# Kernel optimization log

Hardware: AMD Instinct MI355X
Metric: run time of the kernel (lower is better)

## Reference

```python
import jax, jax.numpy as jnp
import numpy as np

TOP_K = 2

def setup_inputs() -> dict:
    key = jax.random.key(0)
    k1, k2 = jax.random.split(key)
    x = jax.random.normal(k1, (8, 4096, 4096), dtype=jnp.float32)
    # nn.Linear weight [num_experts, dim]
    gate_w = jax.random.normal(k2, (64, 4096), dtype=jnp.float32) * (1.0 / np.sqrt(4096))
    return {"x": x, "gate_w": gate_w}

def reference(x, gate_w):
    # logits: [B, S, E]
    logits = jnp.einsum('bsd,ed->bse', x, gate_w)
    routing_weights = jax.nn.softmax(logits, axis=-1)
    top_weights, top_indices = jax.lax.top_k(routing_weights, TOP_K)
    top_weights = top_weights / jnp.sum(top_weights, axis=-1, keepdims=True)
    return top_weights, top_indices
```

## Files before the change

### kernel.cpp

```cpp
#include <hip/hip_runtime.h>
#include <hip/hip_bf16.h>
#include <math.h>


typedef __attribute__((ext_vector_type(8))) short short8;
typedef __attribute__((ext_vector_type(4))) float f32x4;

#define TPB 32
#define NCH 32
#define TAU 1e-4f
#define LROW 68

__device__ __forceinline__ void cvt8(const f32x4* v, short8* hi, short8* lo) {
    const float* f = reinterpret_cast<const float*>(v);
#pragma unroll
    for (int j = 0; j < 8; ++j) {
        __hip_bfloat16 h = __float2bfloat16(f[j]);
        float r = f[j] - __bfloat162float(h);
        __hip_bfloat16 l = __float2bfloat16(r);
        (*hi)[j] = (short)*reinterpret_cast<unsigned short*>(&h);
        (*lo)[j] = (short)*reinterpret_cast<unsigned short*>(&l);
    }
}

__global__ void prep_b(const float* __restrict__ gw,
                       short8* __restrict__ bh, short8* __restrict__ bl) {
    const int tid = blockIdx.x * 256 + threadIdx.x;
    const int ln  = tid & 63;
    const int w   = (tid >> 6) & 127;
    const int nt  = tid >> 13;
    const int row = nt * 16 + (ln & 15);
    const int k   = w * 32 + ((ln >> 4) << 3);
    f32x4 v[2];
    v[0] = *reinterpret_cast<const f32x4*>(gw + (long)row * 4096 + k);
    v[1] = *reinterpret_cast<const f32x4*>(gw + (long)row * 4096 + k + 4);
    short8 h, l;
    cvt8(v, &h, &l);
    bh[tid] = h;
    bl[tid] = l;
}

__device__ __forceinline__ void gload16(const void* g, void* l) {
    __builtin_amdgcn_global_load_lds(
        (const __attribute__((address_space(1))) void*)g,
        (__attribute__((address_space(3))) void*)l, 16, 0, 0);
}

#define STAGE(C, BUF) do {                                                    \
    char* aB = AB + (BUF) * 16384;                                            \
    _Pragma("unroll")                                                         \
    for (int i = 0; i < 4; ++i)                                               \
        gload16(srcA[i] + (long)(C) * 512, aB + (wv * 4 + i) * 1024 + ln * 16); \
} while (0)

__global__ __launch_bounds__(256, 4)
void router_fused(const float* __restrict__ x,
                  const short8* __restrict__ bhp,
                  const short8* __restrict__ blp,
                  const float* __restrict__ gw,
                  float* __restrict__ out,
                  int M, int K) {
    __shared__ __align__(16) char AB[32768];
    __shared__ int flags[TPB];
    __shared__ double Ld4[4][64];

    const int t  = threadIdx.x;
    const int wv = t >> 6;
    const int ln = t & 63;
    const int fr = ln & 15;
    const int q  = ln >> 4;
    const int mm = wv >> 1;
    const int nn = wv & 1;
    const long tok0 = (long)blockIdx.x * TPB;
    const int phase = blockIdx.x & (NCH - 1);

    const char* srcA[4];
#pragma unroll
    for (int i = 0; i < 4; ++i) {
        const int row  = 2 * (wv * 4 + i) + (ln >> 5);
        const int slot = (ln & 31);
        const int swz  = (slot & ~7) | ((slot & 7) ^ (row & 7));
        srcA[i] = (const char*)x + (tok0 + row) * (long)K * 4 + swz * 16;
    }

    f32x4 acc[2];
    acc[0] = (f32x4){0.f, 0.f, 0.f, 0.f};
    acc[1] = (f32x4){0.f, 0.f, 0.f, 0.f};

    STAGE(phase, 0);
    STAGE((phase + 1) & (NCH - 1), 1);

    const int R = mm * 16 + fr;
    const int rk = R & 7;

    for (int j = 0; j < NCH; ++j) {
        const int c   = (phase + j) & (NCH - 1);
        const int buf = j & 1;
        if (j + 1 < NCH) asm volatile("s_waitcnt vmcnt(4)" ::: "memory");
        else             asm volatile("s_waitcnt vmcnt(0)" ::: "memory");
        __builtin_amdgcn_s_barrier();
        asm volatile("" ::: "memory");
        __builtin_amdgcn_sched_barrier(0);

        {
            const char* aB = AB + buf * 16384 + R * 512;
#pragma unroll
            for (int w = 0; w < 4; ++w) {
                f32x4 av[2];
                av[0] = *(const f32x4*)(aB + (w * 8 + ((q * 2 + 0) ^ rk)) * 16);
                av[1] = *(const f32x4*)(aB + (w * 8 + ((q * 2 + 1) ^ rk)) * 16);
                short8 ah, al;
                cvt8(av, &ah, &al);
                const int widx = c * 4 + w;
#pragma unroll
                for (int ntl = 0; ntl < 2; ++ntl) {
                    const int nt = 2 * nn + ntl;
                    short8 bhv = bhp[nt * 8192 + widx * 64 + ln];
                    short8 blv = blp[nt * 8192 + widx * 64 + ln];
                    acc[ntl] = __builtin_amdgcn_mfma_f32_16x16x32_bf16(ah, bhv, acc[ntl], 0, 0, 0);
                    acc[ntl] = __builtin_amdgcn_mfma_f32_16x16x32_bf16(ah, blv, acc[ntl], 0, 0, 0);
                    acc[ntl] = __builtin_amdgcn_mfma_f32_16x16x32_bf16(al, bhv, acc[ntl], 0, 0, 0);
                    acc[ntl] = __builtin_amdgcn_mfma_f32_16x16x32_bf16(al, blv, acc[ntl], 0, 0, 0);
                }
            }
        }

        __builtin_amdgcn_sched_barrier(0);
        asm volatile("" ::: "memory");
        __builtin_amdgcn_s_barrier();
        asm volatile("" ::: "memory");
        if (j + 2 < NCH) STAGE((phase + j + 2) & (NCH - 1), buf);
        __builtin_amdgcn_sched_barrier(0);
    }

    __syncthreads();
    float* Ls = (float*)AB;
#pragma unroll
    for (int ntl = 0; ntl < 2; ++ntl)
#pragma unroll
        for (int r = 0; r < 4; ++r)
            Ls[(mm * 16 + q * 4 + r) * LROW + (2 * nn + ntl) * 16 + fr] = acc[ntl][r];
    __syncthreads();

    if (t < TPB) {
        const float* row = Ls + (long)t * LROW;
        float m1 = -INFINITY, m2 = -INFINITY, m3 = -INFINITY;
        int i1 = 0, i2 = 0;
#pragma unroll 8
        for (int e = 0; e < 64; ++e) {
            const float v = row[e];
            if (v > m1)      { m3 = m2; m2 = m1; i2 = i1; m1 = v; i1 = e; }
            else if (v > m2) { m3 = m2; m2 = v; i2 = e; }
            else if (v > m3) { m3 = v; }
        }
        const float e2 = expf(m2 - m1);
        const float s  = 1.0f + e2;

        const long g = tok0 + t;
        out[2 * g + 0] = 1.0f / s;
        out[2 * g + 1] = e2 / s;
        float* oi = out + 2 * (long)M;
        oi[2 * g + 0] = (float)i1;
        oi[2 * g + 1] = (float)i2;

        flags[t] = ((m1 - m2) < TAU) | ((m2 - m3) < TAU);
    }
    __syncthreads();

    for (int tk = 0; tk < TPB; ++tk) {
        if (flags[tk]) {
            const float* xr = x + (tok0 + tk) * (long)K + wv * 1024;
            const float* gr = gw + (long)ln * (long)K + wv * 1024;
            double s0 = 0.0, s1 = 0.0, s2 = 0.0, s3 = 0.0;
            for (int k = 0; k < 1024; k += 4) {
                const f32x4 a = *reinterpret_cast<const f32x4*>(xr + k);
                const f32x4 b = *reinterpret_cast<const f32x4*>(gr + k);
                s0 = fma((double)a.x, (double)b.x, s0);
                s1 = fma((double)a.y, (double)b.y, s1);
                s2 = fma((double)a.z, (double)b.z, s2);
                s3 = fma((double)a.w, (double)b.w, s3);
            }
            Ld4[wv][ln] = (s0 + s1) + (s2 + s3);
            __syncthreads();
            if (t == 0) {
                double m1 = -INFINITY, m2 = -INFINITY;
                int i1 = 0, i2 = 0;
                for (int e = 0; e < 64; ++e) {
                    const double v = Ld4[0][e] + Ld4[1][e] + Ld4[2][e] + Ld4[3][e];
                    if (v > m1)      { m2 = m1; i2 = i1; m1 = v; i1 = e; }
                    else if (v > m2) { m2 = v; i2 = e; }
                }
                const double e2 = exp(m2 - m1);
                const double s  = 1.0 + e2;
                const long g = tok0 + tk;
                out[2 * g + 0] = (float)(1.0 / s);
                out[2 * g + 1] = (float)(e2 / s);
                float* oi = out + 2 * (long)M;
                oi[2 * g + 0] = (float)i1;
                oi[2 * g + 1] = (float)i2;
            }
            __syncthreads();
        }
    }
}

extern "C" void kernel_launch(void* const* d_in, const int* in_sizes, int n_in,
                              void* d_out, int out_size, void* d_ws, size_t ws_size,
                              hipStream_t stream) {
    const float* x  = (const float*)d_in[0];
    const float* gw = (const float*)d_in[1];
    float* out = (float*)d_out;

    const int K = 4096;
    const int M = in_sizes[0] / K;
    const int nblocks = M / TPB;

    short8* bh = (short8*)d_ws;
    short8* bl = bh + 32768;

    prep_b<<<128, 256, 0, stream>>>(gw, bh, bl);
    router_fused<<<nblocks, 256, 0, stream>>>(x, bh, bl, gw, out, M, K);
}
```

Before: 233.1 us.

## Stage B weights through LDS and widen block to 64 tokens

```diff
diff --git a/kernel.cpp b/kernel.cpp
--- a/kernel.cpp
+++ b/kernel.cpp
@@ -6,8 +6,8 @@
 typedef __attribute__((ext_vector_type(8))) short short8;
 typedef __attribute__((ext_vector_type(4))) float f32x4;
 
-#define TPB 32
-#define NCH 32
+#define TPB 64
+#define NCH 64
 #define TAU 1e-4f
 #define LROW 68
 
@@ -47,20 +47,29 @@
 }
 
 #define STAGE(C, BUF) do {                                                    \
-    char* aB = AB + (BUF) * 16384;                                            \
+    char* aB = AB + (BUF) * 32768;                                            \
+    char* bB = aB + 16384;                                                    \
     _Pragma("unroll")                                                         \
     for (int i = 0; i < 4; ++i)                                               \
-        gload16(srcA[i] + (long)(C) * 512, aB + (wv * 4 + i) * 1024 + ln * 16); \
+        gload16(srcA[i] + (long)(C) * 256, aB + (wv * 4 + i) * 1024 + ln * 16); \
+    _Pragma("unroll")                                                         \
+    for (int i = 0; i < 4; ++i) {                                             \
+        const int s  = wv * 4 + i;                                            \
+        const int wl = s >> 3, nt = (s >> 1) & 3, hl = s & 1;                 \
+        const short8* sp = (hl ? blp : bhp)                                   \
+            + ((long)nt * 8192 + (2 * (C) + wl) * 64 + ln);                   \
+        gload16(sp, bB + s * 1024 + ln * 16);                                 \
+    }                                                                         \
 } while (0)
 
-__global__ __launch_bounds__(256, 4)
+__global__ __launch_bounds__(256, 2)
 void router_fused(const float* __restrict__ x,
                   const short8* __restrict__ bhp,
                   const short8* __restrict__ blp,
                   const float* __restrict__ gw,
                   float* __restrict__ out,
                   int M, int K) {
-    __shared__ __align__(16) char AB[32768];
+    __shared__ __align__(16) char AB[65536];
     __shared__ int flags[TPB];
     __shared__ double Ld4[4][64];
 
@@ -69,58 +78,55 @@
     const int ln = t & 63;
     const int fr = ln & 15;
     const int q  = ln >> 4;
-    const int mm = wv >> 1;
-    const int nn = wv & 1;
     const long tok0 = (long)blockIdx.x * TPB;
     const int phase = blockIdx.x & (NCH - 1);
 
     const char* srcA[4];
 #pragma unroll
     for (int i = 0; i < 4; ++i) {
-        const int row  = 2 * (wv * 4 + i) + (ln >> 5);
-        const int slot = (ln & 31);
-        const int swz  = (slot & ~7) | ((slot & 7) ^ (row & 7));
-        srcA[i] = (const char*)x + (tok0 + row) * (long)K * 4 + swz * 16;
-    }
-
-    f32x4 acc[2];
-    acc[0] = (f32x4){0.f, 0.f, 0.f, 0.f};
-    acc[1] = (f32x4){0.f, 0.f, 0.f, 0.f};
+        const int row  = (wv * 4 + i) * 4 + (ln >> 4);
+        const int sl   = ln & 15;
+        const int lslot = (sl & 8) | ((sl & 7) ^ (row & 7));
+        srcA[i] = (const char*)x + (tok0 + row) * (long)K * 4 + lslot * 16;
+    }
+
+    f32x4 acc[4];
+#pragma unroll
+    for (int nt = 0; nt < 4; ++nt) acc[nt] = (f32x4){0.f, 0.f, 0.f, 0.f};
 
     STAGE(phase, 0);
     STAGE((phase + 1) & (NCH - 1), 1);
 
-    const int R = mm * 16 + fr;
+    const int R  = wv * 16 + fr;
     const int rk = R & 7;
 
     for (int j = 0; j < NCH; ++j) {
         const int c   = (phase + j) & (NCH - 1);
         const int buf = j & 1;
-        if (j + 1 < NCH) asm volatile("s_waitcnt vmcnt(4)" ::: "memory");
+        if (j + 1 < NCH) asm volatile("s_waitcnt vmcnt(8)" ::: "memory");
         else             asm volatile("s_waitcnt vmcnt(0)" ::: "memory");
         __builtin_amdgcn_s_barrier();
         asm volatile("" ::: "memory");
         __builtin_amdgcn_sched_barrier(0);
 
         {
-            const char* aB = AB + buf * 16384 + R * 512;
-#pragma unroll
-            for (int w = 0; w < 4; ++w) {
+            const char* aB = AB + buf * 32768 + R * 256;
+            const char* bB = AB + buf * 32768 + 16384;
+#pragma unroll
+            for (int wl = 0; wl < 2; ++wl) {
                 f32x4 av[2];
-                av[0] = *(const f32x4*)(aB + (w * 8 + ((q * 2 + 0) ^ rk)) * 16);
-                av[1] = *(const f32x4*)(aB + (w * 8 + ((q * 2 + 1) ^ rk)) * 16);
+                av[0] = *(const f32x4*)(aB + (wl * 8 + ((q * 2 + 0) ^ rk)) * 16);
+                av[1] = *(const f32x4*)(aB + (wl * 8 + ((q * 2 + 1) ^ rk)) * 16);
                 short8 ah, al;
                 cvt8(av, &ah, &al);
-                const int widx = c * 4 + w;
-#pragma unroll
-                for (int ntl = 0; ntl < 2; ++ntl) {
-                    const int nt = 2 * nn + ntl;
-                    short8 bhv = bhp[nt * 8192 + widx * 64 + ln];
-                    short8 blv = blp[nt * 8192 + widx * 64 + ln];
-                    acc[ntl] = __builtin_amdgcn_mfma_f32_16x16x32_bf16(ah, bhv, acc[ntl], 0, 0, 0);
-                    acc[ntl] = __builtin_amdgcn_mfma_f32_16x16x32_bf16(ah, blv, acc[ntl], 0, 0, 0);
-                    acc[ntl] = __builtin_amdgcn_mfma_f32_16x16x32_bf16(al, bhv, acc[ntl], 0, 0, 0);
-                    acc[ntl] = __builtin_amdgcn_mfma_f32_16x16x32_bf16(al, blv, acc[ntl], 0, 0, 0);
+#pragma unroll
+                for (int nt = 0; nt < 4; ++nt) {
+                    short8 bhv = *(const short8*)(bB + (wl * 8 + nt * 2 + 0) * 1024 + ln * 16);
+                    short8 blv = *(const short8*)(bB + (wl * 8 + nt * 2 + 1) * 1024 + ln * 16);
+                    acc[nt] = __builtin_amdgcn_mfma_f32_16x16x32_bf16(ah, bhv, acc[nt], 0, 0, 0);
+                    acc[nt] = __builtin_amdgcn_mfma_f32_16x16x32_bf16(ah, blv, acc[nt], 0, 0, 0);
+                    acc[nt] = __builtin_amdgcn_mfma_f32_16x16x32_bf16(al, bhv, acc[nt], 0, 0, 0);
+                    acc[nt] = __builtin_amdgcn_mfma_f32_16x16x32_bf16(al, blv, acc[nt], 0, 0, 0);
                 }
             }
         }
@@ -136,10 +142,10 @@
     __syncthreads();
     float* Ls = (float*)AB;
 #pragma unroll
-    for (int ntl = 0; ntl < 2; ++ntl)
+    for (int nt = 0; nt < 4; ++nt)
 #pragma unroll
         for (int r = 0; r < 4; ++r)
-            Ls[(mm * 16 + q * 4 + r) * LROW + (2 * nn + ntl) * 16 + fr] = acc[ntl][r];
+            Ls[(wv * 16 + q * 4 + r) * LROW + nt * 16 + fr] = acc[nt][r];
     __syncthreads();
 
     if (t < TPB) {
```

New measurement: 206.1 us. 1.13x faster.
